# Kernel optimization log

Hardware: AMD Instinct MI355X
Metric: run time of the kernel (lower is better)

## Reference

```python
import jax, jax.numpy as jnp
import numpy as np

B, C_IN, IMG, P = 64, 3, 224, 16
L, H, E, NC = 12, 12, 768, 1000
HS = E // H          # 64
NSIDE = IMG // P     # 14
NP = NSIDE * NSIDE   # 196
T = NP + 1           # 197 tokens (cls + patches)
EPS = 1e-5


def setup_inputs() -> dict:
    key = jax.random.key(0)
    ks = jax.random.split(key, 16)
    s = 0.02
    inp = {}
    inp["x"] = jax.random.normal(ks[0], (B, C_IN, IMG, IMG), jnp.float32)
    # patch-embed conv (kernel=stride=P) as a linear on flattened patches
    inp["conv_w"] = jax.random.normal(ks[1], (E, C_IN, P, P), jnp.float32) * s
    inp["conv_b"] = jnp.zeros((E,), jnp.float32)
    inp["cls_token"] = jnp.zeros((1, 1, E), jnp.float32)
    inp["pos_embed"] = jax.random.normal(ks[2], (1, T, E), jnp.float32) * s
    # per-layer stacked params, stored in x @ W orientation
    inp["Wq"] = jax.random.normal(ks[3], (L, H, E, HS), jnp.float32) * s
    inp["Wk"] = jax.random.normal(ks[4], (L, H, E, HS), jnp.float32) * s
    inp["Wv"] = jax.random.normal(ks[5], (L, H, E, HS), jnp.float32) * s
    inp["proj_w"] = jax.random.normal(ks[6], (L, E, E), jnp.float32) * s
    inp["proj_b"] = jnp.zeros((L, E), jnp.float32)
    inp["ln1_g"] = jnp.ones((L, E), jnp.float32)
    inp["ln1_b"] = jnp.zeros((L, E), jnp.float32)
    inp["ln2_g"] = jnp.ones((L, E), jnp.float32)
    inp["ln2_b"] = jnp.zeros((L, E), jnp.float32)
    inp["ff1_w"] = jax.random.normal(ks[7], (L, E, 4 * E), jnp.float32) * s
    inp["ff1_b"] = jnp.zeros((L, 4 * E), jnp.float32)
    inp["ff2_w"] = jax.random.normal(ks[8], (L, 4 * E, E), jnp.float32) * s
    inp["ff2_b"] = jnp.zeros((L, E), jnp.float32)
    inp["lnf_g"] = jnp.ones((E,), jnp.float32)
    inp["lnf_b"] = jnp.zeros((E,), jnp.float32)
    inp["head_w"] = jax.random.normal(ks[9], (E, NC), jnp.float32) * s
    inp["head_b"] = jnp.zeros((NC,), jnp.float32)
    return inp


def _layernorm(x, g, b):
    m = x.mean(-1, keepdims=True)
    v = ((x - m) ** 2).mean(-1, keepdims=True)
    return (x - m) / jnp.sqrt(v + EPS) * g + b


def reference(x, conv_w, conv_b, cls_token, pos_embed, Wq, Wk, Wv, proj_w, proj_b,
              ln1_g, ln1_b, ln2_g, ln2_b, ff1_w, ff1_b, ff2_w, ff2_b,
              lnf_g, lnf_b, head_w, head_b):
    b = x.shape[0]
    # --- patch embedding: conv(k=s=P) == linear on flattened (c, ph, pw) patches ---
    xp = x.reshape(b, C_IN, NSIDE, P, NSIDE, P)
    xp = xp.transpose(0, 2, 4, 1, 3, 5).reshape(b, NP, C_IN * P * P)
    tok = xp @ conv_w.reshape(E, -1).T + conv_b  # [b, NP, E]
    cls = jnp.broadcast_to(cls_token, (b, 1, E))
    h = jnp.concatenate([cls, tok], axis=1) + pos_embed  # [b, T, E]

    for i in range(L):
        # --- MTG multi-head attention ---
        xn = _layernorm(h, ln1_g[i], ln1_b[i])
        q = jnp.einsum('btc,hcd->bhtd', xn, Wq[i])
        k = jnp.einsum('btc,hcd->bhtd', xn, Wk[i])
        v = jnp.einsum('btc,hcd->bhtd', xn, Wv[i])
        wei = jnp.einsum('bhtd,bhsd->bhts', q, k) * (HS ** -0.5)
        wei = wei - wei.mean(-1, keepdims=True)           # score centering
        var = (wei * wei).mean(-1, keepdims=True)          # population variance
        wei = jax.nn.softmax(wei / jnp.sqrt(var + EPS), axis=-1)
        attn_out = jnp.einsum('bhts,bhsd->bthd', wei, v).reshape(b, T, E)
        h = h + attn_out @ proj_w[i] + proj_b[i]
        # --- feed-forward ---
        xn2 = _layernorm(h, ln2_g[i], ln2_b[i])
        ff = jax.nn.gelu(xn2 @ ff1_w[i] + ff1_b[i], approximate=False)
        h = h + ff @ ff2_w[i] + ff2_b[i]

    h = _layernorm(h, lnf_g, lnf_b)
    logits = h[:, 0] @ head_w + head_b  # cls token head
    return logits
```

## Files before the change

kernel.cpp:

```cpp
#include <hip/hip_runtime.h>
#include <hip/hip_bf16.h>
#include <cstdint>
#include <cstddef>

typedef __bf16 bf16_t;
typedef __bf16 bf16x8 __attribute__((ext_vector_type(8)));
typedef __bf16 bf16x4 __attribute__((ext_vector_type(4)));
typedef float  f32x4  __attribute__((ext_vector_type(4)));

#define M_TOK 12608
#define M_PAD 12672
#define TPADV 224


__device__ __forceinline__ void gload_lds16(const void* g, void* lds) {
  __builtin_amdgcn_global_load_lds(
      (const __attribute__((address_space(1))) void*)g,
      (__attribute__((address_space(3))) void*)lds, 16, 0, 0);
}

__device__ __forceinline__ float wred64(float v) {
  v += __shfl_xor(v, 32); v += __shfl_xor(v, 16); v += __shfl_xor(v, 8);
  v += __shfl_xor(v, 4);  v += __shfl_xor(v, 2);  v += __shfl_xor(v, 1);
  return v;
}

__device__ __forceinline__ float rowred16(float v) {
  v += __shfl_xor(v, 1); v += __shfl_xor(v, 2);
  v += __shfl_xor(v, 4); v += __shfl_xor(v, 8);
  return v;
}

__device__ __forceinline__ float gelu_fast(float x) {
  const float z = fabsf(x) * 0.70710678118654752f;
  const float t = 1.f / (1.f + 0.3275911f * z);
  const float poly = t * (0.254829592f + t * (-0.284496736f + t * (1.421413741f +
                      t * (-1.453152027f + t * 1.061405429f))));
  const float erfz = 1.f - poly * __expf(-z * z);
  const float erfv = copysignf(erfz, x);
  return 0.5f * x * (1.f + erfv);
}


__global__ void tconv_kernel(const float* __restrict__ in, bf16_t* __restrict__ out,
                             int Kd, int Nd) {
  __shared__ float t[32][33];
  const float* ip = in + (size_t)blockIdx.z * Kd * Nd;
  bf16_t* op = out + (size_t)blockIdx.z * Kd * Nd;
  const int n0 = blockIdx.x * 32, k0 = blockIdx.y * 32;
  const int tx = threadIdx.x, ty = threadIdx.y;
#pragma unroll
  for (int r = 0; r < 32; r += 8)
    t[ty + r][tx] = ip[(size_t)(k0 + ty + r) * Nd + n0 + tx];
  __syncthreads();
#pragma unroll
  for (int r = 0; r < 32; r += 8)
    op[(size_t)(n0 + ty + r) * Kd + k0 + tx] = (bf16_t)t[tx][ty + r];
}

__global__ void qkvconv_kernel(const float* __restrict__ Wq, const float* __restrict__ Wk,
                               const float* __restrict__ Wv, bf16_t* __restrict__ out) {
  __shared__ float t[32][33];
  const int z = blockIdx.z;
  const int li = z / 36, rem = z % 36, which = rem / 12, hh = rem % 12;
  const float* W = (which == 0) ? Wq : ((which == 1) ? Wk : Wv);
  const float* ip = W + (size_t)(li * 12 + hh) * 768 * 64;
  bf16_t* op = out + (size_t)li * 2304 * 768 + (size_t)(which * 768 + hh * 64) * 768;
  const int k0 = blockIdx.x * 32, d0 = blockIdx.y * 32;
  const int tx = threadIdx.x, ty = threadIdx.y;
#pragma unroll
  for (int r = 0; r < 32; r += 8)
    t[ty + r][tx] = ip[(size_t)(k0 + ty + r) * 64 + d0 + tx];
  __syncthreads();
#pragma unroll
  for (int r = 0; r < 32; r += 8)
    op[(size_t)(d0 + ty + r) * 768 + k0 + tx] = (bf16_t)t[tx][ty + r];
}

__global__ void headwconv_kernel(const float* __restrict__ in, bf16_t* __restrict__ out) {
  __shared__ float t[32][33];
  const int n0 = blockIdx.x * 32, k0 = blockIdx.y * 32;
  const int tx = threadIdx.x, ty = threadIdx.y;
#pragma unroll
  for (int r = 0; r < 32; r += 8)
    t[ty + r][tx] = (n0 + tx < 1000) ? in[(size_t)(k0 + ty + r) * 1000 + n0 + tx] : 0.f;
  __syncthreads();
#pragma unroll
  for (int r = 0; r < 32; r += 8)
    out[(size_t)(n0 + ty + r) * 768 + k0 + tx] = (bf16_t)t[tx][ty + r];
}

__global__ void cast_kernel(const float* __restrict__ in, bf16_t* __restrict__ out, int n4) {
  const int id = blockIdx.x * 256 + threadIdx.x;
  if (id >= n4) return;
  float4 v = ((const float4*)in)[id];
  bf16x4 o;
  o[0] = (bf16_t)v.x; o[1] = (bf16_t)v.y; o[2] = (bf16_t)v.z; o[3] = (bf16_t)v.w;
  *(bf16x4*)(out + (size_t)id * 4) = o;
}


__global__ __launch_bounds__(256) void patch_kernel(const float* __restrict__ x,
                                                    bf16_t* __restrict__ xp) {
  const int id = blockIdx.x * 256 + threadIdx.x;
  const int m = id / 48, rem = id % 48;
  const int c = rem >> 4, iy = rem & 15;
  const int pb = m / 196, pp = m - pb * 196;
  const int py = pp / 14, px = pp - py * 14;
  const float4* src = (const float4*)(x + ((size_t)(pb * 3 + c) * 224 + py * 16 + iy) * 224 + px * 16);
  bf16_t* dst = xp + (size_t)m * 768 + c * 256 + iy * 16;
  float4 v0 = src[0], v1 = src[1], v2 = src[2], v3 = src[3];
  bf16x8 o0, o1;
  o0[0] = (bf16_t)v0.x; o0[1] = (bf16_t)v0.y; o0[2] = (bf16_t)v0.z; o0[3] = (bf16_t)v0.w;
  o0[4] = (bf16_t)v1.x; o0[5] = (bf16_t)v1.y; o0[6] = (bf16_t)v1.z; o0[7] = (bf16_t)v1.w;
  o1[0] = (bf16_t)v2.x; o1[1] = (bf16_t)v2.y; o1[2] = (bf16_t)v2.z; o1[3] = (bf16_t)v2.w;
  o1[4] = (bf16_t)v3.x; o1[5] = (bf16_t)v3.y; o1[6] = (bf16_t)v3.z; o1[7] = (bf16_t)v3.w;
  *(bf16x8*)dst = o0;
  *(bf16x8*)(dst + 8) = o1;
}

__global__ void cls_kernel(const float* __restrict__ cls, const float* __restrict__ pos,
                           float* __restrict__ h) {
  const int b = blockIdx.x;
  for (int e = threadIdx.x; e < 768; e += 256)
    h[(size_t)b * 197 * 768 + e] = cls[e] + pos[e];
}

__global__ __launch_bounds__(256) void ln_kernel(const float* __restrict__ h,
    const float* __restrict__ g, const float* __restrict__ bb,
    bf16_t* __restrict__ out, int rows) {
  const int wv = threadIdx.x >> 6, ln = threadIdx.x & 63;
  const int row = blockIdx.x * 4 + wv;
  if (row >= rows) return;
  const float4* hp = (const float4*)(h + (size_t)row * 768);
  float4 xv[3];
  xv[0] = hp[ln]; xv[1] = hp[ln + 64]; xv[2] = hp[ln + 128];
  float s = 0.f;
#pragma unroll
  for (int k = 0; k < 3; ++k) s += xv[k].x + xv[k].y + xv[k].z + xv[k].w;
  s = wred64(s);
  const float mean = s * (1.f / 768.f);
  float vs = 0.f;
#pragma unroll
  for (int k = 0; k < 3; ++k) {
    float a = xv[k].x - mean, b2 = xv[k].y - mean, c = xv[k].z - mean, d = xv[k].w - mean;
    vs += a * a + b2 * b2 + c * c + d * d;
  }
  vs = wred64(vs);
  const float rstd = rsqrtf(vs * (1.f / 768.f) + 1e-5f);
  const float4* gp = (const float4*)g;
  const float4* bp = (const float4*)bb;
  bf16_t* op = out + (size_t)row * 768;
#pragma unroll
  for (int k = 0; k < 3; ++k) {
    const int i4 = ln + 64 * k;
    const float4 gv = gp[i4], bv = bp[i4];
    bf16x4 o;
    o[0] = (bf16_t)((xv[k].x - mean) * rstd * gv.x + bv.x);
    o[1] = (bf16_t)((xv[k].y - mean) * rstd * gv.y + bv.y);
    o[2] = (bf16_t)((xv[k].z - mean) * rstd * gv.z + bv.z);
    o[3] = (bf16_t)((xv[k].w - mean) * rstd * gv.w + bv.w);
    *(bf16x4*)(op + i4 * 4) = o;
  }
}

__global__ __launch_bounds__(256) void lnf_cls_kernel(const float* __restrict__ h,
    const float* __restrict__ g, const float* __restrict__ bb, bf16_t* __restrict__ out) {
  const int wv = threadIdx.x >> 6, ln = threadIdx.x & 63;
  const int b = blockIdx.x * 4 + wv;
  bf16_t* op = out + (size_t)b * 768;
  if (b >= 64) {
    bf16x4 z; z[0] = z[1] = z[2] = z[3] = (bf16_t)0.f;
#pragma unroll
    for (int k = 0; k < 3; ++k) *(bf16x4*)(op + (ln + 64 * k) * 4) = z;
    return;
  }
  const float4* hp = (const float4*)(h + (size_t)b * 197 * 768);
  float4 xv[3];
  xv[0] = hp[ln]; xv[1] = hp[ln + 64]; xv[2] = hp[ln + 128];
  float s = 0.f;
#pragma unroll
  for (int k = 0; k < 3; ++k) s += xv[k].x + xv[k].y + xv[k].z + xv[k].w;
  s = wred64(s);
  const float mean = s * (1.f / 768.f);
  float vs = 0.f;
#pragma unroll
  for (int k = 0; k < 3; ++k) {
    float a = xv[k].x - mean, b2 = xv[k].y - mean, c = xv[k].z - mean, d = xv[k].w - mean;
    vs += a * a + b2 * b2 + c * c + d * d;
  }
  vs = wred64(vs);
  const float rstd = rsqrtf(vs * (1.f / 768.f) + 1e-5f);
  const float4* gp = (const float4*)g;
  const float4* bp = (const float4*)bb;
#pragma unroll
  for (int k = 0; k < 3; ++k) {
    const int i4 = ln + 64 * k;
    const float4 gv = gp[i4], bv = bp[i4];
    bf16x4 o;
    o[0] = (bf16_t)((xv[k].x - mean) * rstd * gv.x + bv.x);
    o[1] = (bf16_t)((xv[k].y - mean) * rstd * gv.y + bv.y);
    o[2] = (bf16_t)((xv[k].z - mean) * rstd * gv.z + bv.z);
    o[3] = (bf16_t)((xv[k].w - mean) * rstd * gv.w + bv.w);
    *(bf16x4*)(op + i4 * 4) = o;
  }
}


enum { EPI_PATCH = 0, EPI_QKV = 1, EPI_BIAS_RES = 2, EPI_GELU = 3, EPI_HEAD = 4 };

template <int EPI>
__global__ __launch_bounds__(256, 3)
void gemm128(const bf16_t* __restrict__ A, const bf16_t* __restrict__ Bt,
             int Mvalid, int K,
             void* __restrict__ out0, const float* __restrict__ bias,
             const float* __restrict__ pos, bf16_t* __restrict__ vtbuf, int ldo) {
  __shared__ __align__(16) bf16_t Al[2][128 * 32];
  __shared__ __align__(16) bf16_t Bl[2][128 * 32];
  const int tid = threadIdx.x;
  const int wv = tid >> 6, ln = tid & 63;
  const int nt = blockIdx.x, mt = blockIdx.y;
  const int wm = wv >> 1, wn = wv & 1;
  const int tl = ln & 15, kg = ln >> 4;
  const int KT = K >> 5;

  const int lr = ln >> 2, lq = ln & 3;
  const int la0 = wv * 32 + lr, la1 = wv * 32 + 16 + lr;
  const int ga0 = lq ^ ((la0 >> 1) & 3), ga1 = lq ^ ((la1 >> 1) & 3);
  const bf16_t* pA0 = A + (size_t)(mt * 128 + la0) * K + ga0 * 8;
  const bf16_t* pA1 = A + (size_t)(mt * 128 + la1) * K + ga1 * 8;
  const bf16_t* pB0 = Bt + (size_t)(nt * 128 + la0) * K + ga0 * 8;
  const bf16_t* pB1 = Bt + (size_t)(nt * 128 + la1) * K + ga1 * 8;
  const int c0 = wv * 1024, c1 = wv * 1024 + 512;

#define STAGE(b_, kt_)                                          \
  { gload_lds16(pA0 + (size_t)(kt_) * 32, &Al[b_][c0]);         \
    gload_lds16(pA1 + (size_t)(kt_) * 32, &Al[b_][c1]);         \
    gload_lds16(pB0 + (size_t)(kt_) * 32, &Bl[b_][c0]);         \
    gload_lds16(pB1 + (size_t)(kt_) * 32, &Bl[b_][c1]); }

  f32x4 acc[4][4];
#pragma unroll
  for (int i = 0; i < 4; ++i)
#pragma unroll
    for (int j = 0; j < 4; ++j) {
      acc[i][j][0] = 0.f; acc[i][j][1] = 0.f; acc[i][j][2] = 0.f; acc[i][j][3] = 0.f;
    }

  STAGE(0, 0);
  __syncthreads();
  for (int kt = 0; kt < KT; ++kt) {
    const int buf = kt & 1;
    if (kt + 1 < KT) STAGE(buf ^ 1, kt + 1);
    bf16x8 af[4], bfr[4];
#pragma unroll
    for (int i = 0; i < 4; ++i) {
      const int ra = wm * 64 + i * 16 + tl;
      af[i] = *(const bf16x8*)(((const char*)&Al[buf][0]) + ra * 64 +
                               (((kg ^ (ra >> 1)) & 3) << 4));
    }
#pragma unroll
    for (int j = 0; j < 4; ++j) {
      const int rb = wn * 64 + j * 16 + tl;
      bfr[j] = *(const bf16x8*)(((const char*)&Bl[buf][0]) + rb * 64 +
                                (((kg ^ (rb >> 1)) & 3) << 4));
    }
    __builtin_amdgcn_s_setprio(1);
#pragma unroll
    for (int i = 0; i < 4; ++i)
#pragma unroll
      for (int j = 0; j < 4; ++j)
        acc[i][j] = __builtin_amdgcn_mfma_f32_16x16x32_bf16(af[i], bfr[j], acc[i][j], 0, 0, 0);
    __builtin_amdgcn_s_setprio(0);
    __syncthreads();
  }
#undef STAGE

  const int mb = mt * 128 + wm * 64, nb = nt * 128 + wn * 64;
#pragma unroll
  for (int i = 0; i < 4; ++i) {
#pragma unroll
    for (int j = 0; j < 4; ++j) {
#pragma unroll
      for (int r = 0; r < 4; ++r) {
        const int m = mb + i * 16 + kg * 4 + r;
        const int n = nb + j * 16 + tl;
        if (m >= Mvalid) continue;
        const float v = acc[i][j][r];
        if constexpr (EPI == EPI_PATCH) {
          const int pb = m / 196, pp = m - pb * 196;
          const float val = v + bias[n] + pos[(size_t)(pp + 1) * 768 + n];
          ((float*)out0)[(size_t)(m + pb + 1) * 768 + n] = val;
        } else if constexpr (EPI == EPI_QKV) {
          if (n < 1536) {
            ((bf16_t*)out0)[(size_t)m * 1536 + n] = (bf16_t)v;
          } else {
            const int hh2 = (n - 1536) >> 6, dd = n & 63;
            const int pb = m / 197, tt = m - pb * 197;
            vtbuf[((size_t)(pb * 12 + hh2) * 64 + dd) * TPADV + tt] = (bf16_t)v;
          }
        } else if constexpr (EPI == EPI_BIAS_RES) {
          float* hp = (float*)out0 + (size_t)m * 768 + n;
          *hp += v + bias[n];
        } else if constexpr (EPI == EPI_HEAD) {
          if (n < 1000)
            ((float*)out0)[(size_t)m * 1000 + n] = v + bias[n];
        } else {
          ((bf16_t*)out0)[(size_t)m * (size_t)ldo + n] = (bf16_t)gelu_fast(v + bias[n]);
        }
      }
    }
  }
}

__global__ __launch_bounds__(256, 2)
void attn_kernel(const bf16_t* __restrict__ qk, const bf16_t* __restrict__ vt,
                 bf16_t* __restrict__ attno) {
  __shared__ bf16_t Kl[224 * 72];
  __shared__ bf16_t Pl[4][16 * 232];
  const int bh = blockIdx.x;
  const int b = bh / 12, hh = bh % 12;
  const int tid = threadIdx.x, wv = tid >> 6, ln = tid & 63;
  const int tl = ln & 15, kg = ln >> 4;

  for (int idx = tid; idx < 224 * 8; idx += 256) {
    const int s = idx >> 3, c = idx & 7;
    bf16x8 val;
    if (s < 197) {
      val = *(const bf16x8*)(qk + (size_t)(b * 197 + s) * 1536 + 768 + hh * 64 + c * 8);
    } else {
#pragma unroll
      for (int j2 = 0; j2 < 8; ++j2) val[j2] = (bf16_t)0.f;
    }
    *(bf16x8*)&Kl[s * 72 + c * 8] = val;
  }
  __syncthreads();

  for (int qt = wv; qt < 13; qt += 4) {
    const size_t qoff = (size_t)(b * 197 + qt * 16 + tl) * 1536 + hh * 64 + kg * 8;
    const bf16x8 aq0 = *(const bf16x8*)(qk + qoff);
    const bf16x8 aq1 = *(const bf16x8*)(qk + qoff + 32);
    f32x4 sc[13];
#pragma unroll
    for (int st = 0; st < 13; ++st) {
      const bf16x8 bk0 = *(const bf16x8*)&Kl[(st * 16 + tl) * 72 + kg * 8];
      const bf16x8 bk1 = *(const bf16x8*)&Kl[(st * 16 + tl) * 72 + 32 + kg * 8];
      f32x4 z = {0.f, 0.f, 0.f, 0.f};
      z = __builtin_amdgcn_mfma_f32_16x16x32_bf16(aq0, bk0, z, 0, 0, 0);
      z = __builtin_amdgcn_mfma_f32_16x16x32_bf16(aq1, bk1, z, 0, 0, 0);
      sc[st] = z;
    }
#pragma unroll
    for (int st = 0; st < 13; ++st)
#pragma unroll
      for (int r = 0; r < 4; ++r) sc[st][r] *= 0.125f;

    float inv[4];
#pragma unroll
    for (int r = 0; r < 4; ++r) {
      float sum = 0.f;
#pragma unroll
      for (int st = 0; st < 13; ++st)
        if (st * 16 + tl < 197) sum += sc[st][r];
      sum = rowred16(sum);
      const float mean = sum * (1.f / 197.f);
      float ss = 0.f;
#pragma unroll
      for (int st = 0; st < 13; ++st)
        if (st * 16 + tl < 197) { const float cc = sc[st][r] - mean; ss += cc * cc; }
      ss = rowred16(ss);
      const float rstd = rsqrtf(ss * (1.f / 197.f) + 1e-5f);
      float ps = 0.f;
#pragma unroll
      for (int st = 0; st < 13; ++st) {
        const int s = st * 16 + tl;
        float p = 0.f;
        if (s < 197) p = __expf((sc[st][r] - mean) * rstd);
        ps += p;
        Pl[wv][(kg * 4 + r) * 232 + st * 16 + tl] = (bf16_t)p;
      }
      ps = rowred16(ps);
      inv[r] = 1.f / ps;
      Pl[wv][(kg * 4 + r) * 232 + 208 + tl] = (bf16_t)0.f;
      if (tl < 8) Pl[wv][(kg * 4 + r) * 232 + 224 + tl] = (bf16_t)0.f;
    }

    f32x4 oa[4];
#pragma unroll
    for (int nf = 0; nf < 4; ++nf) {
      oa[nf][0] = 0.f; oa[nf][1] = 0.f; oa[nf][2] = 0.f; oa[nf][3] = 0.f;
    }
#pragma unroll
    for (int kk = 0; kk < 7; ++kk) {
      const bf16x8 pa = *(const bf16x8*)&Pl[wv][tl * 232 + kk * 32 + kg * 8];
#pragma unroll
      for (int nf = 0; nf < 4; ++nf) {
        const bf16x8 vb = *(const bf16x8*)(vt + ((size_t)bh * 64 + nf * 16 + tl) * TPADV + kk * 32 + kg * 8);
        oa[nf] = __builtin_amdgcn_mfma_f32_16x16x32_bf16(pa, vb, oa[nf], 0, 0, 0);
      }
    }
#pragma unroll
    for (int nf = 0; nf < 4; ++nf)
#pragma unroll
      for (int r = 0; r < 4; ++r) {
        const int t = qt * 16 + kg * 4 + r;
        if (t < 197)
          attno[(size_t)(b * 197 + t) * 768 + hh * 64 + nf * 16 + tl] =
              (bf16_t)(oa[nf][r] * inv[r]);
      }
  }
}


extern "C" void kernel_launch(void* const* d_in, const int* in_sizes, int n_in,
                              void* d_out, int out_size, void* d_ws, size_t ws_size,
                              hipStream_t stream) {
  (void)in_sizes; (void)n_in; (void)out_size; (void)ws_size;
  const float* x      = (const float*)d_in[0];
  const float* conv_w = (const float*)d_in[1];
  const float* conv_b = (const float*)d_in[2];
  const float* cls_t  = (const float*)d_in[3];
  const float* pos    = (const float*)d_in[4];
  const float* Wq     = (const float*)d_in[5];
  const float* Wk     = (const float*)d_in[6];
  const float* Wv     = (const float*)d_in[7];
  const float* proj_w = (const float*)d_in[8];
  const float* proj_b = (const float*)d_in[9];
  const float* ln1_g  = (const float*)d_in[10];
  const float* ln1_b  = (const float*)d_in[11];
  const float* ln2_g  = (const float*)d_in[12];
  const float* ln2_b  = (const float*)d_in[13];
  const float* ff1_w  = (const float*)d_in[14];
  const float* ff1_b  = (const float*)d_in[15];
  const float* ff2_w  = (const float*)d_in[16];
  const float* ff2_b  = (const float*)d_in[17];
  const float* lnf_g  = (const float*)d_in[18];
  const float* lnf_b  = (const float*)d_in[19];
  const float* head_w = (const float*)d_in[20];
  const float* head_b = (const float*)d_in[21];
  float* out = (float*)d_out;

  char* w = (char*)d_ws;
  size_t off = 0;
  auto take = [&](size_t bytes) {
    char* p = w + off;
    off = (off + bytes + 255) & ~(size_t)255;
    return p;
  };
  bf16_t* Wc_t    = (bf16_t*)take((size_t)768 * 768 * 2);
  bf16_t* Wqkv_t  = (bf16_t*)take((size_t)12 * 2304 * 768 * 2);
  bf16_t* Wproj_t = (bf16_t*)take((size_t)12 * 768 * 768 * 2);
  bf16_t* Wff1_t  = (bf16_t*)take((size_t)12 * 3072 * 768 * 2);
  bf16_t* Wff2_t  = (bf16_t*)take((size_t)12 * 768 * 3072 * 2);
  bf16_t* Wht     = (bf16_t*)take((size_t)1024 * 768 * 2);
  float*  hbuf    = (float*)take((size_t)M_PAD * 768 * 4);
  bf16_t* xn      = (bf16_t*)take((size_t)M_PAD * 768 * 2);
  bf16_t* qkb     = (bf16_t*)take((size_t)M_PAD * 1536 * 2);
  bf16_t* vtb     = (bf16_t*)take((size_t)768 * 64 * TPADV * 2);
  bf16_t* attno   = (bf16_t*)take((size_t)M_PAD * 768 * 2);
  bf16_t* ffa     = (bf16_t*)take((size_t)M_PAD * 3072 * 2);
  bf16_t* xcls    = (bf16_t*)take((size_t)256 * 768 * 2);

  const dim3 blk256(256);
  const dim3 tb(32, 8);

  tconv_kernel<<<dim3(24, 24, 12), tb, 0, stream>>>(proj_w, Wproj_t, 768, 768);
  tconv_kernel<<<dim3(96, 24, 12), tb, 0, stream>>>(ff1_w, Wff1_t, 768, 3072);
  tconv_kernel<<<dim3(24, 96, 12), tb, 0, stream>>>(ff2_w, Wff2_t, 3072, 768);
  qkvconv_kernel<<<dim3(24, 2, 432), tb, 0, stream>>>(Wq, Wk, Wv, Wqkv_t);
  headwconv_kernel<<<dim3(32, 24), tb, 0, stream>>>(head_w, Wht);
  cast_kernel<<<dim3(576), blk256, 0, stream>>>(conv_w, Wc_t, 147456);

  patch_kernel<<<dim3(2352), blk256, 0, stream>>>(x, xn);
  cls_kernel<<<dim3(64), blk256, 0, stream>>>(cls_t, pos, hbuf);
  gemm128<EPI_PATCH><<<dim3(6, 98), blk256, 0, stream>>>(
      xn, Wc_t, 12544, 768, (void*)hbuf, conv_b, pos, (bf16_t*)nullptr, 768);

  for (int i = 0; i < 12; ++i) {
    ln_kernel<<<dim3(3152), blk256, 0, stream>>>(hbuf, ln1_g + i * 768, ln1_b + i * 768, xn, M_TOK);
    gemm128<EPI_QKV><<<dim3(18, 99), blk256, 0, stream>>>(
        xn, Wqkv_t + (size_t)i * 2304 * 768, M_TOK, 768, (void*)qkb,
        (const float*)nullptr, (const float*)nullptr, vtb, 1536);
    attn_kernel<<<dim3(768), blk256, 0, stream>>>(qkb, vtb, attno);
    gemm128<EPI_BIAS_RES><<<dim3(6, 99), blk256, 0, stream>>>(
        attno, Wproj_t + (size_t)i * 768 * 768, M_TOK, 768, (void*)hbuf,
        proj_b + i * 768, (const float*)nullptr, (bf16_t*)nullptr, 768);
    ln_kernel<<<dim3(3152), blk256, 0, stream>>>(hbuf, ln2_g + i * 768, ln2_b + i * 768, xn, M_TOK);
    gemm128<EPI_GELU><<<dim3(24, 99), blk256, 0, stream>>>(
        xn, Wff1_t + (size_t)i * 768 * 3072, M_TOK, 768, (void*)ffa,
        ff1_b + i * 3072, (const float*)nullptr, (bf16_t*)nullptr, 3072);
    gemm128<EPI_BIAS_RES><<<dim3(6, 99), blk256, 0, stream>>>(
        ffa, Wff2_t + (size_t)i * 3072 * 768, M_TOK, 3072, (void*)hbuf,
        ff2_b + i * 768, (const float*)nullptr, (bf16_t*)nullptr, 768);
  }

  lnf_cls_kernel<<<dim3(64), blk256, 0, stream>>>(hbuf, lnf_g, lnf_b, xcls);
  gemm128<EPI_HEAD><<<dim3(8, 2), blk256, 0, stream>>>(
      xcls, Wht, 64, 768, (void*)out, head_b, (const float*)nullptr,
      (bf16_t*)nullptr, 1000);
}
```

Baseline: 5.381 ms.

## Triple-buffer GEMM LDS tiles with explicit vmcnt waits to keep loads in flight

The 128x128 bf16 GEMM now uses three LDS stages instead of two. Each k-step issues the global-to-LDS load for two tiles ahead, then uses a partial s_waitcnt vmcnt(4) plus a raw barrier instead of __syncthreads, so one tile's loads stay outstanding while the current tile is computed. The loop is unrolled by three with rotating buffer indices, and out-of-range prefetches are clamped to the last tile. This costs 50% more shared memory per block, which can hurt occupancy. It also assumes the K-tile count is a multiple of three and at least two.

```diff
diff --git a/kernel.cpp b/kernel.cpp
--- a/kernel.cpp
+++ b/kernel.cpp
@@ -215,8 +215,8 @@
              int Mvalid, int K,
              void* __restrict__ out0, const float* __restrict__ bias,
              const float* __restrict__ pos, bf16_t* __restrict__ vtbuf, int ldo) {
-  __shared__ __align__(16) bf16_t Al[2][128 * 32];
-  __shared__ __align__(16) bf16_t Bl[2][128 * 32];
+  __shared__ __align__(16) bf16_t Al[3][128 * 32];
+  __shared__ __align__(16) bf16_t Bl[3][128 * 32];
   const int tid = threadIdx.x;
   const int wv = tid >> 6, ln = tid & 63;
   const int nt = blockIdx.x, mt = blockIdx.y;
@@ -247,34 +247,43 @@
       acc[i][j][0] = 0.f; acc[i][j][1] = 0.f; acc[i][j][2] = 0.f; acc[i][j][3] = 0.f;
     }
 
+#define KSTEP(bc_, bs_, ktn_)                                               \
+  {                                                                         \
+    const int skt = ((ktn_) < KT) ? (ktn_) : (KT - 1);                      \
+    STAGE(bs_, skt);                                                        \
+    bf16x8 af[4], bfr[4];                                                   \
+    _Pragma("unroll") for (int i = 0; i < 4; ++i) {                         \
+      const int ra = wm * 64 + i * 16 + tl;                                 \
+      af[i] = *(const bf16x8*)(((const char*)&Al[bc_][0]) + ra * 64 +       \
+                               (((kg ^ (ra >> 1)) & 3) << 4));              \
+    }                                                                       \
+    _Pragma("unroll") for (int j = 0; j < 4; ++j) {                         \
+      const int rb = wn * 64 + j * 16 + tl;                                 \
+      bfr[j] = *(const bf16x8*)(((const char*)&Bl[bc_][0]) + rb * 64 +      \
+                                (((kg ^ (rb >> 1)) & 3) << 4));             \
+    }                                                                       \
+    __builtin_amdgcn_s_setprio(1);                                          \
+    _Pragma("unroll") for (int i = 0; i < 4; ++i)                           \
+      _Pragma("unroll") for (int j = 0; j < 4; ++j)                         \
+        acc[i][j] = __builtin_amdgcn_mfma_f32_16x16x32_bf16(                \
+            af[i], bfr[j], acc[i][j], 0, 0, 0);                             \
+    __builtin_amdgcn_s_setprio(0);                                          \
+    asm volatile("s_waitcnt vmcnt(4) lgkmcnt(0)" ::: "memory");             \
+    __builtin_amdgcn_s_barrier();                                           \
+  }
+
   STAGE(0, 0);
-  __syncthreads();
-  for (int kt = 0; kt < KT; ++kt) {
-    const int buf = kt & 1;
-    if (kt + 1 < KT) STAGE(buf ^ 1, kt + 1);
-    bf16x8 af[4], bfr[4];
-#pragma unroll
-    for (int i = 0; i < 4; ++i) {
-      const int ra = wm * 64 + i * 16 + tl;
-      af[i] = *(const bf16x8*)(((const char*)&Al[buf][0]) + ra * 64 +
-                               (((kg ^ (ra >> 1)) & 3) << 4));
-    }
-#pragma unroll
-    for (int j = 0; j < 4; ++j) {
-      const int rb = wn * 64 + j * 16 + tl;
-      bfr[j] = *(const bf16x8*)(((const char*)&Bl[buf][0]) + rb * 64 +
-                                (((kg ^ (rb >> 1)) & 3) << 4));
-    }
-    __builtin_amdgcn_s_setprio(1);
-#pragma unroll
-    for (int i = 0; i < 4; ++i)
-#pragma unroll
-      for (int j = 0; j < 4; ++j)
-        acc[i][j] = __builtin_amdgcn_mfma_f32_16x16x32_bf16(af[i], bfr[j], acc[i][j], 0, 0, 0);
-    __builtin_amdgcn_s_setprio(0);
-    __syncthreads();
+  STAGE(1, 1);
+  asm volatile("s_waitcnt vmcnt(4)" ::: "memory");
+  __builtin_amdgcn_s_barrier();
+
+  for (int kt = 0; kt < KT; kt += 3) {
+    KSTEP(0, 2, kt + 2);
+    KSTEP(1, 0, kt + 3);
+    KSTEP(2, 1, kt + 4);
   }
 #undef STAGE
+#undef KSTEP
 
   const int mb = mt * 128 + wm * 64, nb = nt * 128 + wn * 64;
 #pragma unroll
```

Measured after the change: 5.771 ms. 1.07x slower.
